# Optimization experiments

Measured on AMD Instinct MI355X. Metric: run time of the kernel, lower is better.

Reference implementation:

```python
import jax, jax.numpy as jnp
import numpy as np

NEG_BIG = -10000000000.0  # value used by masked_fill_ in the original


def setup_inputs() -> dict:
    S, B, H = 2048, 16, 1024
    key = jax.random.key(0)
    ks = jax.random.split(key, 6)
    return {
        "hidden": jax.random.normal(ks[0], (1, B, H), dtype=jnp.float32),
        "hidden_sequence": jax.random.normal(ks[1], (S, B, H), dtype=jnp.float32),
        "input_masks": jax.random.randint(ks[2], (S, B), 0, 2) > 0,
        "W_att": jax.random.normal(ks[3], (H, 2 * H), dtype=jnp.float32) * (1.0 / np.sqrt(2 * H)),
        "b_att": jax.random.normal(ks[4], (H,), dtype=jnp.float32) * 0.01,
        "v": jax.random.normal(ks[5], (H,), dtype=jnp.float32),
    }


def reference(hidden, hidden_sequence, input_masks, W_att, b_att, v):
    S, B, H = hidden_sequence.shape
    # concat score: tanh(Linear([hidden; hidden_seq])) . v  -> [S, B]
    h = jnp.broadcast_to(hidden, (S, B, H))
    concat_hidden = jnp.concatenate([h, hidden_sequence], axis=2)  # [S, B, 2H]
    energy = jnp.tanh(jnp.einsum('sbk,hk->sbh', concat_hidden, W_att) + b_att)
    score = jnp.einsum('sbh,h->sb', energy, v)  # [S, B]
    # masked_fill_(~mask, -1e10); the original's .permute(1,0) result is discarded
    score = jnp.where(input_masks, score, jnp.float32(NEG_BIG))
    # faithful: softmax over dim=1 of the [S, B] energy (as in the source)
    attention_weight = jax.nn.softmax(score, axis=1)  # [S, B]
    # bmm([B,1,S], [B,S,H]) -> [B,1,H] -> permute(1,0,2) -> [1,B,H]
    context = jnp.einsum('sb,sbh->bh', attention_weight, hidden_sequence)[None, :, :]
    return context
```

## Files before the change

kernel.cpp:

```cpp
#include <hip/hip_runtime.h>
#include <math.h>

#define S_LEN 2048
#define B_SZ  16
#define H_SZ  1024
#define M_SZ  32768

typedef __attribute__((ext_vector_type(8))) _Float16 half8;
typedef __attribute__((ext_vector_type(4))) float f32x4;

__device__ __forceinline__ unsigned pack2h(float a, float b) {
    _Float16 ha = (_Float16)a, hb = (_Float16)b;
    unsigned short ua = __builtin_bit_cast(unsigned short, ha);
    unsigned short ub = __builtin_bit_cast(unsigned short, hb);
    return (unsigned)ua | ((unsigned)ub << 16);
}

__device__ __forceinline__ int phys_off(int r, int sl) {
    return ((r >> 1) << 7) + ((((r & 1) << 2 | sl) ^ ((r >> 1) & 7)) << 4);
}

__device__ __forceinline__ void dma16(const void* g, void* l) {
    __builtin_amdgcn_global_load_lds(
        (const __attribute__((address_space(1))) unsigned int*)g,
        (__attribute__((address_space(3))) unsigned int*)l, 16, 0, 0);
}

__global__ void k_hidden_part(const float* __restrict__ hidden,
                              const float* __restrict__ W,
                              const float* __restrict__ b_att,
                              float* __restrict__ hp) {
    int gid  = blockIdx.x * blockDim.x + threadIdx.x;
    int wave = gid >> 6;
    int lane = threadIdx.x & 63;
    int b = wave >> 10;
    int h = wave & 1023;
    const float* x = hidden + b * H_SZ;
    const float* w = W + (size_t)h * (2 * H_SZ);
    float acc = 0.f;
    #pragma unroll
    for (int k = 0; k < H_SZ; k += 64) acc += x[k + lane] * w[k + lane];
    #pragma unroll
    for (int off = 32; off; off >>= 1) acc += __shfl_down(acc, off, 64);
    if (lane == 0) hp[b * H_SZ + h] = acc + b_att[h];
}

__global__ void k_convw(const float* __restrict__ W,
                        unsigned short* __restrict__ Wsw) {
    int t = blockIdx.x * 256 + threadIdx.x;
    int sl = t & 3, r = (t >> 2) & 127, kt = (t >> 9) & 31, nt = t >> 14;
    const float* src = W + (size_t)(nt * 128 + r) * 2048 + 1024 + kt * 32 + sl * 8;
    float4 f0 = *(const float4*)src;
    float4 f1 = *(const float4*)(src + 4);
    uint4 u;
    u.x = pack2h(f0.x, f0.y); u.y = pack2h(f0.z, f0.w);
    u.z = pack2h(f1.x, f1.y); u.w = pack2h(f1.z, f1.w);
    *(uint4*)((char*)Wsw + (size_t)(nt * 32 + kt) * 8192 + phys_off(r, sl)) = u;
}

#define SA    0
#define SB    8192
#define SBUF  16384

__global__ __launch_bounds__(256, 3)
void k_score_dma(const float* __restrict__ X,
                 const unsigned short* __restrict__ Wsw,
                 const float* __restrict__ hp,
                 const float* __restrict__ v,
                 float* __restrict__ score_part) {
    __shared__ char lds[2 * SBUF];

    const int t = threadIdx.x;
    int wg = (blockIdx.x & 7) * 256 + (blockIdx.x >> 3);
    const int m0 = (wg >> 3) * 128;
    const int nt = wg & 7;
    const int n0 = nt * 128;

    const int lane = t & 63, wid = t >> 6;
    const int wm = wid >> 1, wn = wid & 1;
    const int lr = lane & 15, lq = lane >> 4;

    const int srow = t >> 1, shalf = t & 1;
    const float* Xp = X + (size_t)(m0 + srow) * 1024 + shalf * 16;
    const int aOff0 = phys_off(srow, shalf * 2 + 0);
    const int aOff1 = phys_off(srow, shalf * 2 + 1);

    const unsigned short* Bp = Wsw + (size_t)(nt * 32) * 4096 + wid * 1024 + lane * 8;

    int aro[4], bro[4];
    #pragma unroll
    for (int i = 0; i < 4; ++i) {
        aro[i] = phys_off(wm * 64 + i * 16 + lr, lq);
        bro[i] = phys_off(wn * 64 + i * 16 + lr, lq);
    }

    f32x4 acc[4][4];
    #pragma unroll
    for (int i = 0; i < 4; ++i)
        #pragma unroll
        for (int j = 0; j < 4; ++j) acc[i][j] = (f32x4)0.f;

    float4 ax[4];

#define LOADA(kt)                                                              \
    {                                                                          \
        const float* p = Xp + (kt) * 32;                                       \
        ax[0] = *(const float4*)(p);                                           \
        ax[1] = *(const float4*)(p + 4);                                       \
        ax[2] = *(const float4*)(p + 8);                                       \
        ax[3] = *(const float4*)(p + 12);                                      \
    }

#define DMAB(bufbase, kt)                                                      \
    {                                                                          \
        const unsigned short* s0 = Bp + (size_t)(kt) * 4096;                   \
        dma16(s0,       (bufbase) + SB + wid * 2048);                          \
        dma16(s0 + 512, (bufbase) + SB + wid * 2048 + 1024);                   \
    }

#define STAGEA(bufbase)                                                        \
    {                                                                          \
        uint4 p0, p1;                                                          \
        p0.x = pack2h(ax[0].x, ax[0].y); p0.y = pack2h(ax[0].z, ax[0].w);      \
        p0.z = pack2h(ax[1].x, ax[1].y); p0.w = pack2h(ax[1].z, ax[1].w);      \
        p1.x = pack2h(ax[2].x, ax[2].y); p1.y = pack2h(ax[2].z, ax[2].w);      \
        p1.z = pack2h(ax[3].x, ax[3].y); p1.w = pack2h(ax[3].z, ax[3].w);      \
        *(uint4*)((bufbase) + SA + aOff0) = p0;                                \
        *(uint4*)((bufbase) + SA + aOff1) = p1;                                \
    }

    LOADA(0);
    DMAB(lds, 0);
    STAGEA(lds);
    __syncthreads();

    for (int kt = 0; kt < 32; ++kt) {
        char* cur = lds + (kt & 1) * SBUF;
        char* nxt = lds + ((kt & 1) ^ 1) * SBUF;
        if (kt < 31) {
            LOADA(kt + 1);
            DMAB(nxt, kt + 1);
        }

        half8 ah[4], bh[4];
        #pragma unroll
        for (int i = 0; i < 4; ++i) ah[i] = *(const half8*)(cur + SA + aro[i]);
        #pragma unroll
        for (int j = 0; j < 4; ++j) bh[j] = *(const half8*)(cur + SB + bro[j]);

        #pragma unroll
        for (int i = 0; i < 4; ++i)
            #pragma unroll
            for (int j = 0; j < 4; ++j)
                acc[i][j] = __builtin_amdgcn_mfma_f32_16x16x32_f16(ah[i], bh[j], acc[i][j], 0, 0, 0);

        if (kt < 31) STAGEA(nxt);
        __syncthreads();
    }

    float* red = (float*)lds;
    #pragma unroll
    for (int i = 0; i < 4; ++i) {
        #pragma unroll
        for (int r = 0; r < 4; ++r) {
            const int b = lq * 4 + r;
            float s = 0.f;
            #pragma unroll
            for (int j = 0; j < 4; ++j) {
                const int c = n0 + wn * 64 + j * 16 + lr;
                s += v[c] * tanhf(acc[i][j][r] + hp[b * H_SZ + c]);
            }
            s += __shfl_xor(s, 1);
            s += __shfl_xor(s, 2);
            s += __shfl_xor(s, 4);
            s += __shfl_xor(s, 8);
            if (lr == 0)
                red[wn * 128 + wm * 64 + i * 16 + lq * 4 + r] = s;
        }
    }
    __syncthreads();
    if (t < 128)
        score_part[nt * M_SZ + m0 + t] = red[t] + red[128 + t];
#undef LOADA
#undef DMAB
#undef STAGEA
}

__global__ __launch_bounds__(256)
void k_context_sm(const float* __restrict__ part,
                  const int* __restrict__ masks,
                  const float* __restrict__ X,
                  float* __restrict__ partial) {
    __shared__ float wlds[64];

    const int t = threadIdx.x;
    const int b = blockIdx.x & 15;
    const int c = blockIdx.x >> 4;

    if (t < 64) {
        const int s = c * 64 + t;
        float vals[16];
        float mx = -INFINITY;
        #pragma unroll
        for (int bb = 0; bb < 16; ++bb) {
            const int m = s * 16 + bb;
            float sc = 0.f;
            #pragma unroll
            for (int p = 0; p < 8; ++p) sc += part[p * M_SZ + m];
            sc = masks[m] ? sc : -1e10f;
            vals[bb] = sc;
            mx = fmaxf(mx, sc);
        }
        float sum = 0.f;
        #pragma unroll
        for (int bb = 0; bb < 16; ++bb) { vals[bb] = __expf(vals[bb] - mx); sum += vals[bb]; }
        wlds[t] = vals[b] / sum;
    }
    __syncthreads();

    const int h = t * 4;
    float4 acc = make_float4(0.f, 0.f, 0.f, 0.f);
    #pragma unroll 4
    for (int i = 0; i < 64; ++i) {
        float w = wlds[i];
        float4 x = *(const float4*)(X + ((size_t)((c * 64 + i) * 16 + b)) * 1024 + h);
        acc.x += w * x.x; acc.y += w * x.y; acc.z += w * x.z; acc.w += w * x.w;
    }
    *(float4*)(partial + (size_t)(c * 16 + b) * 1024 + h) = acc;
}

__global__ void k_context_reduce(const float* __restrict__ partial,
                                 float* __restrict__ out) {
    int o = blockIdx.x * blockDim.x + threadIdx.x;
    int b = o >> 10, h = o & 1023;
    float s = 0.f;
    #pragma unroll
    for (int cc = 0; cc < 32; ++cc) s += partial[(size_t)(cc * 16 + b) * 1024 + h];
    out[o] = s;
}

extern "C" void kernel_launch(void* const* d_in, const int* in_sizes, int n_in,
                              void* d_out, int out_size, void* d_ws, size_t ws_size,
                              hipStream_t stream) {
    const float* hidden = (const float*)d_in[0];
    const float* hseq   = (const float*)d_in[1];
    const int*   masks  = (const int*)d_in[2];
    const float* W      = (const float*)d_in[3];
    const float* b_att  = (const float*)d_in[4];
    const float* v      = (const float*)d_in[5];
    float* out = (float*)d_out;

    float* wsf        = (float*)d_ws;
    float* hp         = wsf;
    float* score_part = wsf + 16384;
    float* partial    = score_part + 8 * M_SZ;
    unsigned short* Wsw = (unsigned short*)(partial + 32 * 16 * 1024);

    hipLaunchKernelGGL(k_hidden_part,    dim3(4096), dim3(256), 0, stream, hidden, W, b_att, hp);
    hipLaunchKernelGGL(k_convw,          dim3(512),  dim3(256), 0, stream, W, Wsw);
    hipLaunchKernelGGL(k_score_dma,      dim3(2048), dim3(256), 0, stream, hseq, Wsw, hp, v, score_part);
    hipLaunchKernelGGL(k_context_sm,     dim3(512),  dim3(256), 0, stream, score_part, masks, hseq, partial);
    hipLaunchKernelGGL(k_context_reduce, dim3(64),   dim3(256), 0, stream, partial, out);
}
```

Measured before the change: 382.8 us.

## Pre-convert hidden sequence to swizzled fp16 tiles and DMA both GEMM operands

Adds a pre-pass that converts the fp32 hidden sequence into swizzled fp16 tiles in workspace. The score GEMM can then load both A and B straight into LDS with global_load_lds, with no register staging or packing. Occupancy rises to 4 blocks per CU, and the softmax is split out of the context kernel into its own kernel with larger context chunks. The cost is an extra full pass that reads 128MB fp32 and writes 64MB fp16, plus a fallback path when the workspace is too small.

```diff
diff --git a/kernel.cpp b/kernel.cpp
--- a/kernel.cpp
+++ b/kernel.cpp
@@ -45,34 +45,36 @@
     if (lane == 0) hp[b * H_SZ + h] = acc + b_att[h];
 }
 
-__global__ void k_convw(const float* __restrict__ W,
-                        unsigned short* __restrict__ Wsw) {
+__global__ void k_conv_tiles(const float* __restrict__ src,
+                             unsigned short* __restrict__ dst,
+                             int rowStride, int colOff) {
     int t = blockIdx.x * 256 + threadIdx.x;
-    int sl = t & 3, r = (t >> 2) & 127, kt = (t >> 9) & 31, nt = t >> 14;
-    const float* src = W + (size_t)(nt * 128 + r) * 2048 + 1024 + kt * 32 + sl * 8;
-    float4 f0 = *(const float4*)src;
-    float4 f1 = *(const float4*)(src + 4);
+    int sl = t & 3, r = (t >> 2) & 127, kt = (t >> 9) & 31, p = t >> 14;
+    const float* s = src + (size_t)(p * 128 + r) * rowStride + colOff + kt * 32 + sl * 8;
+    float4 f0 = *(const float4*)s;
+    float4 f1 = *(const float4*)(s + 4);
     uint4 u;
     u.x = pack2h(f0.x, f0.y); u.y = pack2h(f0.z, f0.w);
     u.z = pack2h(f1.x, f1.y); u.w = pack2h(f1.z, f1.w);
-    *(uint4*)((char*)Wsw + (size_t)(nt * 32 + kt) * 8192 + phys_off(r, sl)) = u;
-}
-
-#define SA    0
-#define SB    8192
-#define SBUF  16384
-
-__global__ __launch_bounds__(256, 3)
-void k_score_dma(const float* __restrict__ X,
-                 const unsigned short* __restrict__ Wsw,
-                 const float* __restrict__ hp,
-                 const float* __restrict__ v,
-                 float* __restrict__ score_part) {
-    __shared__ char lds[2 * SBUF];
+    *(uint4*)((char*)dst + (size_t)(p * 32 + kt) * 8192 + phys_off(r, sl)) = u;
+}
+
+#define SA2   0
+#define SB2   8192
+#define SBUF2 16384
+
+__global__ __launch_bounds__(256, 4)
+void k_score_dma2(const unsigned short* __restrict__ Xsw,
+                  const unsigned short* __restrict__ Wsw,
+                  const float* __restrict__ hp,
+                  const float* __restrict__ v,
+                  float* __restrict__ score_part) {
+    __shared__ char lds[2 * SBUF2];
 
     const int t = threadIdx.x;
     int wg = (blockIdx.x & 7) * 256 + (blockIdx.x >> 3);
-    const int m0 = (wg >> 3) * 128;
+    const int mp = wg >> 3;
+    const int m0 = mp * 128;
     const int nt = wg & 7;
     const int n0 = nt * 128;
 
@@ -80,12 +82,8 @@
     const int wm = wid >> 1, wn = wid & 1;
     const int lr = lane & 15, lq = lane >> 4;
 
-    const int srow = t >> 1, shalf = t & 1;
-    const float* Xp = X + (size_t)(m0 + srow) * 1024 + shalf * 16;
-    const int aOff0 = phys_off(srow, shalf * 2 + 0);
-    const int aOff1 = phys_off(srow, shalf * 2 + 1);
-
-    const unsigned short* Bp = Wsw + (size_t)(nt * 32) * 4096 + wid * 1024 + lane * 8;
+    const char* At = (const char*)Xsw + (size_t)mp * 32 * 8192 + wid * 1024 + lane * 16;
+    const char* Bt = (const char*)Wsw + (size_t)nt * 32 * 8192 + wid * 1024 + lane * 16;
 
     int aro[4], bro[4];
     #pragma unroll
@@ -100,53 +98,29 @@
         #pragma unroll
         for (int j = 0; j < 4; ++j) acc[i][j] = (f32x4)0.f;
 
-    float4 ax[4];
-
-#define LOADA(kt)                                                              \
+#define DMA2(bufbase, kt)                                                      \
     {                                                                          \
-        const float* p = Xp + (kt) * 32;                                       \
-        ax[0] = *(const float4*)(p);                                           \
-        ax[1] = *(const float4*)(p + 4);                                       \
-        ax[2] = *(const float4*)(p + 8);                                       \
-        ax[3] = *(const float4*)(p + 12);                                      \
-    }
-
-#define DMAB(bufbase, kt)                                                      \
-    {                                                                          \
-        const unsigned short* s0 = Bp + (size_t)(kt) * 4096;                   \
-        dma16(s0,       (bufbase) + SB + wid * 2048);                          \
-        dma16(s0 + 512, (bufbase) + SB + wid * 2048 + 1024);                   \
-    }
-
-#define STAGEA(bufbase)                                                        \
-    {                                                                          \
-        uint4 p0, p1;                                                          \
-        p0.x = pack2h(ax[0].x, ax[0].y); p0.y = pack2h(ax[0].z, ax[0].w);      \
-        p0.z = pack2h(ax[1].x, ax[1].y); p0.w = pack2h(ax[1].z, ax[1].w);      \
-        p1.x = pack2h(ax[2].x, ax[2].y); p1.y = pack2h(ax[2].z, ax[2].w);      \
-        p1.z = pack2h(ax[3].x, ax[3].y); p1.w = pack2h(ax[3].z, ax[3].w);      \
-        *(uint4*)((bufbase) + SA + aOff0) = p0;                                \
-        *(uint4*)((bufbase) + SA + aOff1) = p1;                                \
-    }
-
-    LOADA(0);
-    DMAB(lds, 0);
-    STAGEA(lds);
+        const char* a = At + (size_t)(kt) * 8192;                              \
+        const char* b = Bt + (size_t)(kt) * 8192;                              \
+        dma16(a,        (bufbase) + SA2 + wid * 1024);                         \
+        dma16(a + 4096, (bufbase) + SA2 + 4096 + wid * 1024);                  \
+        dma16(b,        (bufbase) + SB2 + wid * 1024);                         \
+        dma16(b + 4096, (bufbase) + SB2 + 4096 + wid * 1024);                  \
+    }
+
+    DMA2(lds, 0);
     __syncthreads();
 
     for (int kt = 0; kt < 32; ++kt) {
-        char* cur = lds + (kt & 1) * SBUF;
-        char* nxt = lds + ((kt & 1) ^ 1) * SBUF;
-        if (kt < 31) {
-            LOADA(kt + 1);
-            DMAB(nxt, kt + 1);
-        }
+        char* cur = lds + (kt & 1) * SBUF2;
+        char* nxt = lds + ((kt & 1) ^ 1) * SBUF2;
+        if (kt < 31) DMA2(nxt, kt + 1);
 
         half8 ah[4], bh[4];
         #pragma unroll
-        for (int i = 0; i < 4; ++i) ah[i] = *(const half8*)(cur + SA + aro[i]);
-        #pragma unroll
-        for (int j = 0; j < 4; ++j) bh[j] = *(const half8*)(cur + SB + bro[j]);
+        for (int i = 0; i < 4; ++i) ah[i] = *(const half8*)(cur + SA2 + aro[i]);
+        #pragma unroll
+        for (int j = 0; j < 4; ++j) bh[j] = *(const half8*)(cur + SB2 + bro[j]);
 
         #pragma unroll
         for (int i = 0; i < 4; ++i)
@@ -154,7 +128,6 @@
             for (int j = 0; j < 4; ++j)
                 acc[i][j] = __builtin_amdgcn_mfma_f32_16x16x32_f16(ah[i], bh[j], acc[i][j], 0, 0, 0);
 
-        if (kt < 31) STAGEA(nxt);
         __syncthreads();
     }
 
@@ -181,49 +154,168 @@
     __syncthreads();
     if (t < 128)
         score_part[nt * M_SZ + m0 + t] = red[t] + red[128 + t];
+#undef DMA2
+}
+
+__global__ __launch_bounds__(256, 3)
+void k_score_dma(const float* __restrict__ X,
+                 const unsigned short* __restrict__ Wsw,
+                 const float* __restrict__ hp,
+                 const float* __restrict__ v,
+                 float* __restrict__ score_part) {
+    __shared__ char lds[2 * SBUF2];
+
+    const int t = threadIdx.x;
+    int wg = (blockIdx.x & 7) * 256 + (blockIdx.x >> 3);
+    const int m0 = (wg >> 3) * 128;
+    const int nt = wg & 7;
+    const int n0 = nt * 128;
+
+    const int lane = t & 63, wid = t >> 6;
+    const int wm = wid >> 1, wn = wid & 1;
+    const int lr = lane & 15, lq = lane >> 4;
+
+    const int srow = t >> 1, shalf = t & 1;
+    const float* Xp = X + (size_t)(m0 + srow) * 1024 + shalf * 16;
+    const int aOff0 = phys_off(srow, shalf * 2 + 0);
+    const int aOff1 = phys_off(srow, shalf * 2 + 1);
+
+    const unsigned short* Bp = Wsw + (size_t)(nt * 32) * 4096 + wid * 512 + lane * 8;
+
+    int aro[4], bro[4];
+    #pragma unroll
+    for (int i = 0; i < 4; ++i) {
+        aro[i] = phys_off(wm * 64 + i * 16 + lr, lq);
+        bro[i] = phys_off(wn * 64 + i * 16 + lr, lq);
+    }
+
+    f32x4 acc[4][4];
+    #pragma unroll
+    for (int i = 0; i < 4; ++i)
+        #pragma unroll
+        for (int j = 0; j < 4; ++j) acc[i][j] = (f32x4)0.f;
+
+    float4 ax[4];
+
+#define LOADA(kt)                                                              \
+    {                                                                          \
+        const float* p = Xp + (kt) * 32;                                       \
+        ax[0] = *(const float4*)(p);                                           \
+        ax[1] = *(const float4*)(p + 4);                                       \
+        ax[2] = *(const float4*)(p + 8);                                       \
+        ax[3] = *(const float4*)(p + 12);                                      \
+    }
+
+#define DMAB(bufbase, kt)                                                      \
+    {                                                                          \
+        const unsigned short* s0 = Bp + (size_t)(kt) * 4096;                   \
+        dma16(s0,        (bufbase) + SB2 + wid * 1024);                        \
+        dma16(s0 + 2048, (bufbase) + SB2 + wid * 1024 + 4096);                 \
+    }
+
+#define STAGEA(bufbase)                                                        \
+    {                                                                          \
+        uint4 p0, p1;                                                          \
+        p0.x = pack2h(ax[0].x, ax[0].y); p0.y = pack2h(ax[0].z, ax[0].w);      \
+        p0.z = pack2h(ax[1].x, ax[1].y); p0.w = pack2h(ax[1].z, ax[1].w);      \
+        p1.x = pack2h(ax[2].x, ax[2].y); p1.y = pack2h(ax[2].z, ax[2].w);      \
+        p1.z = pack2h(ax[3].x, ax[3].y); p1.w = pack2h(ax[3].z, ax[3].w);      \
+        *(uint4*)((bufbase) + SA2 + aOff0) = p0;                               \
+        *(uint4*)((bufbase) + SA2 + aOff1) = p1;                               \
+    }
+
+    LOADA(0);
+    DMAB(lds, 0);
+    STAGEA(lds);
+    __syncthreads();
+
+    for (int kt = 0; kt < 32; ++kt) {
+        char* cur = lds + (kt & 1) * SBUF2;
+        char* nxt = lds + ((kt & 1) ^ 1) * SBUF2;
+        if (kt < 31) {
+            LOADA(kt + 1);
+            DMAB(nxt, kt + 1);
+        }
+
+        half8 ah[4], bh[4];
+        #pragma unroll
+        for (int i = 0; i < 4; ++i) ah[i] = *(const half8*)(cur + SA2 + aro[i]);
+        #pragma unroll
+        for (int j = 0; j < 4; ++j) bh[j] = *(const half8*)(cur + SB2 + bro[j]);
+
+        #pragma unroll
+        for (int i = 0; i < 4; ++i)
+            #pragma unroll
+            for (int j = 0; j < 4; ++j)
+                acc[i][j] = __builtin_amdgcn_mfma_f32_16x16x32_f16(ah[i], bh[j], acc[i][j], 0, 0, 0);
+
+        if (kt < 31) STAGEA(nxt);
+        __syncthreads();
+    }
+
+    float* red = (float*)lds;
+    #pragma unroll
+    for (int i = 0; i < 4; ++i) {
+        #pragma unroll
+        for (int r = 0; r < 4; ++r) {
+            const int b = lq * 4 + r;
+            float s = 0.f;
+            #pragma unroll
+            for (int j = 0; j < 4; ++j) {
+                const int c = n0 + wn * 64 + j * 16 + lr;
+                s += v[c] * tanhf(acc[i][j][r] + hp[b * H_SZ + c]);
+            }
+            s += __shfl_xor(s, 1);
+            s += __shfl_xor(s, 2);
+            s += __shfl_xor(s, 4);
+            s += __shfl_xor(s, 8);
+            if (lr == 0)
+                red[wn * 128 + wm * 64 + i * 16 + lq * 4 + r] = s;
+        }
+    }
+    __syncthreads();
+    if (t < 128)
+        score_part[nt * M_SZ + m0 + t] = red[t] + red[128 + t];
 #undef LOADA
 #undef DMAB
 #undef STAGEA
 }
 
-__global__ __launch_bounds__(256)
-void k_context_sm(const float* __restrict__ part,
-                  const int* __restrict__ masks,
-                  const float* __restrict__ X,
-                  float* __restrict__ partial) {
-    __shared__ float wlds[64];
-
-    const int t = threadIdx.x;
-    const int b = blockIdx.x & 15;
-    const int c = blockIdx.x >> 4;
-
-    if (t < 64) {
-        const int s = c * 64 + t;
-        float vals[16];
-        float mx = -INFINITY;
-        #pragma unroll
-        for (int bb = 0; bb < 16; ++bb) {
-            const int m = s * 16 + bb;
-            float sc = 0.f;
-            #pragma unroll
-            for (int p = 0; p < 8; ++p) sc += part[p * M_SZ + m];
-            sc = masks[m] ? sc : -1e10f;
-            vals[bb] = sc;
-            mx = fmaxf(mx, sc);
-        }
-        float sum = 0.f;
-        #pragma unroll
-        for (int bb = 0; bb < 16; ++bb) { vals[bb] = __expf(vals[bb] - mx); sum += vals[bb]; }
-        wlds[t] = vals[b] / sum;
-    }
-    __syncthreads();
-
-    const int h = t * 4;
+__global__ void k_softmax(const float* __restrict__ part,
+                          const int* __restrict__ masks,
+                          float* __restrict__ wts) {
+    int s = blockIdx.x * blockDim.x + threadIdx.x;
+    if (s >= S_LEN) return;
+    float vals[16];
+    float mx = -INFINITY;
+    #pragma unroll
+    for (int b = 0; b < 16; ++b) {
+        int m = s * 16 + b;
+        float sc = 0.f;
+        #pragma unroll
+        for (int p = 0; p < 8; ++p) sc += part[p * M_SZ + m];
+        sc = masks[m] ? sc : -1e10f;
+        vals[b] = sc;
+        mx = fmaxf(mx, sc);
+    }
+    float sum = 0.f;
+    #pragma unroll
+    for (int b = 0; b < 16; ++b) { vals[b] = __expf(vals[b] - mx); sum += vals[b]; }
+    float inv = 1.f / sum;
+    #pragma unroll
+    for (int b = 0; b < 16; ++b) wts[s * 16 + b] = vals[b] * inv;
+}
+
+__global__ void k_context_partial(const float* __restrict__ wts,
+                                  const float* __restrict__ X,
+                                  float* __restrict__ partial) {
+    int b = blockIdx.x & 15;
+    int c = blockIdx.x >> 4;
+    int h = threadIdx.x * 4;
     float4 acc = make_float4(0.f, 0.f, 0.f, 0.f);
-    #pragma unroll 4
-    for (int i = 0; i < 64; ++i) {
-        float w = wlds[i];
-        float4 x = *(const float4*)(X + ((size_t)((c * 64 + i) * 16 + b)) * 1024 + h);
+    for (int s = c * 128; s < c * 128 + 128; ++s) {
+        float w = wts[s * 16 + b];
+        float4 x = *(const float4*)(X + (size_t)(s * 16 + b) * 1024 + h);
         acc.x += w * x.x; acc.y += w * x.y; acc.z += w * x.z; acc.w += w * x.w;
     }
     *(float4*)(partial + (size_t)(c * 16 + b) * 1024 + h) = acc;
@@ -235,7 +327,7 @@
     int b = o >> 10, h = o & 1023;
     float s = 0.f;
     #pragma unroll
-    for (int cc = 0; cc < 32; ++cc) s += partial[(size_t)(cc * 16 + b) * 1024 + h];
+    for (int cc = 0; cc < 16; ++cc) s += partial[(size_t)(cc * 16 + b) * 1024 + h];
     out[o] = s;
 }
 
@@ -252,13 +344,23 @@
 
     float* wsf        = (float*)d_ws;
     float* hp         = wsf;
-    float* score_part = wsf + 16384;
+    float* wts        = wsf + 16384;
+    float* score_part = wts + 32768;
     float* partial    = score_part + 8 * M_SZ;
-    unsigned short* Wsw = (unsigned short*)(partial + 32 * 16 * 1024);
-
-    hipLaunchKernelGGL(k_hidden_part,    dim3(4096), dim3(256), 0, stream, hidden, W, b_att, hp);
-    hipLaunchKernelGGL(k_convw,          dim3(512),  dim3(256), 0, stream, W, Wsw);
-    hipLaunchKernelGGL(k_score_dma,      dim3(2048), dim3(256), 0, stream, hseq, Wsw, hp, v, score_part);
-    hipLaunchKernelGGL(k_context_sm,     dim3(512),  dim3(256), 0, stream, score_part, masks, hseq, partial);
-    hipLaunchKernelGGL(k_context_reduce, dim3(64),   dim3(256), 0, stream, partial, out);
-}
+    unsigned short* Wsw = (unsigned short*)(partial + 262144);
+    unsigned short* Xsw = (unsigned short*)((char*)Wsw + 2 * 1024 * 1024);
+    const size_t WS_FAST = (size_t)(16384 + 32768 + 262144 + 262144) * 4
+                         + 2ull * 1024 * 1024 + 64ull * 1024 * 1024;
+
+    hipLaunchKernelGGL(k_hidden_part, dim3(4096), dim3(256), 0, stream, hidden, W, b_att, hp);
+    hipLaunchKernelGGL(k_conv_tiles,  dim3(512),  dim3(256), 0, stream, W, Wsw, 2048, 1024);
+    if (ws_size >= WS_FAST) {
+        hipLaunchKernelGGL(k_conv_tiles,  dim3(16384), dim3(256), 0, stream, hseq, Xsw, 1024, 0);
+        hipLaunchKernelGGL(k_score_dma2,  dim3(2048),  dim3(256), 0, stream, Xsw, Wsw, hp, v, score_part);
+    } else {
+        hipLaunchKernelGGL(k_score_dma,   dim3(2048),  dim3(256), 0, stream, hseq, Wsw, hp, v, score_part);
+    }
+    hipLaunchKernelGGL(k_softmax,         dim3(8),   dim3(256), 0, stream, score_part, masks, wts);
+    hipLaunchKernelGGL(k_context_partial, dim3(256), dim3(256), 0, stream, wts, hseq, partial);
+    hipLaunchKernelGGL(k_context_reduce,  dim3(64),  dim3(256), 0, stream, partial, out);
+}
```

Result: faster. 359.1 us (-6.2%).
